# Performance work log

Measured on AMD Instinct MI355X. Metric: run time of the kernel, lower is better.

The kernel has to match this reference:

```python
import jax, jax.numpy as jnp
import numpy as np

B, T, DIM = 8, 2048, 512
DM, EXPAND, NSTATE, HDIM, L = 128, 2, 16, 64, 2
DINNER = DM * EXPAND            # 256
NH = DINNER // HDIM             # 4 heads
CONVDIM = DINNER + 2 * NSTATE   # 288 (n_groups=1)
PROJ = DINNER + CONVDIM + NH    # 548
K = 4                           # conv kernel (HF default)
EPS = 1e-5


def setup_inputs() -> dict:
    key = jax.random.key(0)
    ks = jax.random.split(key, 8)
    s = 0.02
    return {
        "x": jax.random.normal(ks[0], (B, T, DIM), jnp.float32),
        "in_w": jax.random.normal(ks[1], (DIM, DM), jnp.float32) * s,
        "in_b": jnp.zeros((DM,), jnp.float32),
        "norm_w": jnp.ones((L, DM), jnp.float32),
        "inproj_w": jax.random.normal(ks[2], (L, DM, PROJ), jnp.float32) * s,
        "conv_w": jax.random.normal(ks[3], (L, CONVDIM, 1, K), jnp.float32) * 0.2,
        "conv_b": jnp.zeros((L, CONVDIM), jnp.float32),
        "A_log": jnp.log(jax.random.uniform(ks[4], (L, NH), jnp.float32, 1.0, 8.0)),
        "D": jnp.ones((L, NH), jnp.float32),
        "dt_bias": jnp.log(jnp.expm1(jax.random.uniform(ks[5], (L, NH), jnp.float32, 1e-3, 0.1))),
        "gnorm_w": jnp.ones((L, DINNER), jnp.float32),
        "outproj_w": jax.random.normal(ks[6], (L, DINNER, DM), jnp.float32) * s,
        "normf_w": jnp.ones((DM,), jnp.float32),
        "out_w": jax.random.normal(ks[7], (DM, DIM), jnp.float32) * s,
        "out_b": jnp.zeros((DIM,), jnp.float32),
    }


def _rmsnorm(x, w):
    var = jnp.mean(x * x, axis=-1, keepdims=True)
    return x * jax.lax.rsqrt(var + EPS) * w


def _gated_rmsnorm(y, gate, w):
    y = y * jax.nn.silu(gate)
    var = jnp.mean(y * y, axis=-1, keepdims=True)
    return y * jax.lax.rsqrt(var + EPS) * w


def _causal_conv(h, w, b):
    # h: [B,T,C] depthwise causal conv, kernel K, left pad K-1
    out = jax.lax.conv_general_dilated(
        h.swapaxes(1, 2), w, (1,), [(K - 1, 0)],
        feature_group_count=CONVDIM,
        dimension_numbers=("NCH", "OIH", "NCH"))
    return out.swapaxes(1, 2) + b


def _ssd(xs, dt, A, Bm, Cm, Dh):
    # selective state-space scan (math-equivalent to HF Mamba2 chunked SSD)
    # xs [B,T,H,P], dt [B,T,H], A [H], Bm/Cm [B,T,N], Dh [H]
    dA = jnp.exp(dt * A)  # [B,T,H]

    def step(state, inp):
        dA_t, dt_t, x_t, B_t, C_t = inp
        dBx = dt_t[:, :, None, None] * x_t[..., None] * B_t[:, None, None, :]
        state = state * dA_t[:, :, None, None] + dBx  # [B,H,P,N]
        y = jnp.einsum("bhpn,bn->bhp", state, C_t)
        return state, y

    init = jnp.zeros((xs.shape[0], NH, HDIM, NSTATE), xs.dtype)
    _, ys = jax.lax.scan(step, init, (dA.swapaxes(0, 1), dt.swapaxes(0, 1),
                                      xs.swapaxes(0, 1), Bm.swapaxes(0, 1), Cm.swapaxes(0, 1)))
    return ys.swapaxes(0, 1) + xs * Dh[None, None, :, None]


def reference(x, in_w, in_b, norm_w, inproj_w, conv_w, conv_b, A_log, D,
              dt_bias, gnorm_w, outproj_w, normf_w, out_w, out_b):
    h = x @ in_w + in_b  # [B,T,DM]
    for l in range(L):
        res = h
        hn = _rmsnorm(h, norm_w[l])
        proj = hn @ inproj_w[l]  # [B,T,PROJ]
        gate = proj[..., :DINNER]
        hBC = proj[..., DINNER:DINNER + CONVDIM]
        dt = proj[..., DINNER + CONVDIM:]
        hBC = jax.nn.silu(_causal_conv(hBC, conv_w[l], conv_b[l]))
        xs = hBC[..., :DINNER].reshape(B, T, NH, HDIM)
        Bm = hBC[..., DINNER:DINNER + NSTATE]
        Cm = hBC[..., DINNER + NSTATE:]
        A = -jnp.exp(A_log[l])
        dt = jax.nn.softplus(dt + dt_bias[l])  # time_step_limit=(0,inf): no clamp
        y = _ssd(xs, dt, A, Bm, Cm, D[l]).reshape(B, T, DINNER)
        y = _gated_rmsnorm(y, gate, gnorm_w[l])
        h = res + y @ outproj_w[l]
    h = _rmsnorm(h, normf_w)
    pooled = h.mean(axis=1)  # mean pool over T
    return pooled @ out_w + out_b
```

## Files before the change

### kernel.cpp

```cpp
#include <hip/hip_runtime.h>
#include <math.h>

typedef unsigned short ushort_t;
typedef unsigned int uint_t;

#define B_      8
#define T_      2048
#define DIMX    512
#define DM      128
#define DINNER  256
#define NSTATE  16
#define HDIM    64
#define NH      4
#define CONVDIM 288
#define PROJ    548
#define KCONV   4
#define LLAYERS 2
#define QCH     128
#define NC      (T_/QCH)
#define EPSF    1e-5f
#define MTOK    (B_*T_)

#define OFF_H      0u
#define OFF_PROJ   2097152u
#define OFF_HBC    11075584u
#define OFF_Y      15794176u
#define OFF_DTP    19988480u
#define OFF_CUM    20054016u
#define OFF_Z      20119552u
#define OFF_SPREV  20643840u
#define OFF_DEC    21168128u
#define OFF_PART   21168640u
#define OFF_BF     21299712u
#define OFF_WTIN   23396864u
#define OFF_WTINP  23429632u
#define OFF_WTOUT  23503360u

__device__ __forceinline__ ushort_t f2b(float f) {
    uint_t u = __builtin_bit_cast(uint_t, f);
    return (ushort_t)((u + 0x7FFFu + ((u >> 16) & 1u)) >> 16);
}
__device__ __forceinline__ float b2f(ushort_t b) {
    uint_t u = ((uint_t)b) << 16;
    return __builtin_bit_cast(float, u);
}

typedef short bf8 __attribute__((ext_vector_type(8)));
typedef float f4v __attribute__((ext_vector_type(4)));

__global__ __launch_bounds__(256) void k_wt_all(
    const float* __restrict__ in_w, const float* __restrict__ inproj_w,
    const float* __restrict__ outproj_w,
    ushort_t* __restrict__ wt_in, ushort_t* __restrict__ wt_inp,
    ushort_t* __restrict__ wt_out)
{
    __shared__ float tile[64][65];
    int idx = blockIdx.x;
    const float* W; ushort_t* Wt; int K, N, k0, n0;
    if (idx < 16) {
        W = in_w; Wt = wt_in; K = 512; N = 128;
        k0 = (idx & 7) * 64; n0 = (idx >> 3) * 64;
    } else if (idx < 52) {
        int r = idx - 16; int l = r / 18; r -= l * 18;
        W = inproj_w + l * 128 * PROJ; Wt = wt_inp + l * 576 * 128; K = 128; N = PROJ;
        k0 = (r & 1) * 64; n0 = (r >> 1) * 64;
    } else {
        int r = idx - 52; int l = r / 8; r -= l * 8;
        W = outproj_w + l * 256 * 128; Wt = wt_out + l * 128 * 256; K = 256; N = 128;
        k0 = (r & 3) * 64; n0 = (r >> 2) * 64;
    }
    const int tid = threadIdx.x;
#pragma unroll
    for (int it = 0; it < 16; ++it) {
        const int e = it * 256 + tid;
        const int kk = e >> 6, nn = e & 63;
        tile[kk][nn] = (n0 + nn < N) ? W[(k0 + kk) * N + (n0 + nn)] : 0.f;
    }
    __syncthreads();
#pragma unroll
    for (int it = 0; it < 16; ++it) {
        const int e = it * 256 + tid;
        const int nn = e >> 6, kk = e & 63;
        Wt[(n0 + nn) * K + k0 + kk] = f2b(tile[kk][nn]);
    }
}

template<int KTOT, int LDC, int NGUARD, int EPI, bool ABF16>
__global__ __launch_bounds__(256) void k_gemm(
    const void* __restrict__ Ap, const ushort_t* __restrict__ Bt,
    const float* __restrict__ aux, float* __restrict__ C)
{
    __shared__ ushort_t Als[64 * 136];
    __shared__ ushort_t Bls[64 * 136];
    const int m0 = blockIdx.x * 64, n0 = blockIdx.y * 64;
    const int tid = threadIdx.x;
    const int lane = tid & 63, w = tid >> 6;
    const int wm = (w >> 1) * 32, wn = (w & 1) * 32;
    const int r16 = lane & 15, q8 = (lane >> 4) * 8;

    f4v acc[2][2];
#pragma unroll
    for (int i = 0; i < 2; ++i)
#pragma unroll
        for (int j = 0; j < 2; ++j) acc[i][j] = (f4v)0.f;

    for (int kc = 0; kc < KTOT; kc += 128) {
        if constexpr (ABF16) {
            const ushort_t* A = (const ushort_t*)Ap;
#pragma unroll
            for (int i = 0; i < 4; ++i) {
                const int e = i * 2048 + tid * 8;
                const int r = e >> 7, c = e & 127;
                *(uint4*)&Als[r * 136 + c] = *(const uint4*)&A[(m0 + r) * KTOT + kc + c];
            }
        } else {
            const float* A = (const float*)Ap;
#pragma unroll
            for (int i = 0; i < 4; ++i) {
                const int e = i * 2048 + tid * 8;
                const int r = e >> 7, c = e & 127;
                const float4 f0 = *(const float4*)&A[(m0 + r) * KTOT + kc + c];
                const float4 f1 = *(const float4*)&A[(m0 + r) * KTOT + kc + c + 4];
                uint4 pk;
                pk.x = (uint_t)f2b(f0.x) | ((uint_t)f2b(f0.y) << 16);
                pk.y = (uint_t)f2b(f0.z) | ((uint_t)f2b(f0.w) << 16);
                pk.z = (uint_t)f2b(f1.x) | ((uint_t)f2b(f1.y) << 16);
                pk.w = (uint_t)f2b(f1.z) | ((uint_t)f2b(f1.w) << 16);
                *(uint4*)&Als[r * 136 + c] = pk;
            }
        }
#pragma unroll
        for (int i = 0; i < 4; ++i) {
            const int e = i * 2048 + tid * 8;
            const int r = e >> 7, c = e & 127;
            *(uint4*)&Bls[r * 136 + c] = *(const uint4*)&Bt[(n0 + r) * KTOT + kc + c];
        }
        __syncthreads();
#pragma unroll
        for (int kk = 0; kk < 128; kk += 32) {
            const bf8 a0 = *(const bf8*)&Als[(wm + r16) * 136 + kk + q8];
            const bf8 a1 = *(const bf8*)&Als[(wm + 16 + r16) * 136 + kk + q8];
            const bf8 b0 = *(const bf8*)&Bls[(wn + r16) * 136 + kk + q8];
            const bf8 b1 = *(const bf8*)&Bls[(wn + 16 + r16) * 136 + kk + q8];
            acc[0][0] = __builtin_amdgcn_mfma_f32_16x16x32_bf16(a0, b0, acc[0][0], 0, 0, 0);
            acc[0][1] = __builtin_amdgcn_mfma_f32_16x16x32_bf16(a0, b1, acc[0][1], 0, 0, 0);
            acc[1][0] = __builtin_amdgcn_mfma_f32_16x16x32_bf16(a1, b0, acc[1][0], 0, 0, 0);
            acc[1][1] = __builtin_amdgcn_mfma_f32_16x16x32_bf16(a1, b1, acc[1][1], 0, 0, 0);
        }
        __syncthreads();
    }
    const int q4 = (lane >> 4) * 4;
#pragma unroll
    for (int i = 0; i < 2; ++i)
#pragma unroll
        for (int j = 0; j < 2; ++j)
#pragma unroll
            for (int r = 0; r < 4; ++r) {
                const int grow = m0 + wm + i * 16 + q4 + r;
                const int gcol = n0 + wn + j * 16 + r16;
                if (NGUARD == 0 || gcol < NGUARD) {
                    float v = acc[i][j][r];
                    if (EPI == 1) v += aux[gcol];
                    if (EPI == 2) v += C[grow * LDC + gcol];
                    C[grow * LDC + gcol] = v;
                }
            }
}

__global__ __launch_bounds__(256) void k_gemm_rms(
    const float* __restrict__ h, const float* __restrict__ nw,
    const ushort_t* __restrict__ Bt, float* __restrict__ C)
{
    __shared__ ushort_t Als[64 * 136];
    __shared__ ushort_t Bls[64 * 136];
    const int m0 = blockIdx.x * 64, n0 = blockIdx.y * 64;
    const int tid = threadIdx.x;
    const int lane = tid & 63, w = tid >> 6;
    const int wm = (w >> 1) * 32, wn = (w & 1) * 32;
    const int r16 = lane & 15, q8 = (lane >> 4) * 8;

#pragma unroll
    for (int i = 0; i < 4; ++i) {
        const int e = i * 2048 + tid * 8;
        const int r = e >> 7, c = e & 127;
        const float4 f0 = *(const float4*)&h[(m0 + r) * 128 + c];
        const float4 f1 = *(const float4*)&h[(m0 + r) * 128 + c + 4];
        float ss = f0.x * f0.x + f0.y * f0.y + f0.z * f0.z + f0.w * f0.w
                 + f1.x * f1.x + f1.y * f1.y + f1.z * f1.z + f1.w * f1.w;
#pragma unroll
        for (int off = 1; off < 16; off <<= 1) ss += __shfl_xor(ss, off);
        const float rs = rsqrtf(ss * (1.f / 128.f) + EPSF);
        const float4 w0 = *(const float4*)&nw[c];
        const float4 w1 = *(const float4*)&nw[c + 4];
        uint4 pk;
        pk.x = (uint_t)f2b(f0.x * rs * w0.x) | ((uint_t)f2b(f0.y * rs * w0.y) << 16);
        pk.y = (uint_t)f2b(f0.z * rs * w0.z) | ((uint_t)f2b(f0.w * rs * w0.w) << 16);
        pk.z = (uint_t)f2b(f1.x * rs * w1.x) | ((uint_t)f2b(f1.y * rs * w1.y) << 16);
        pk.w = (uint_t)f2b(f1.z * rs * w1.z) | ((uint_t)f2b(f1.w * rs * w1.w) << 16);
        *(uint4*)&Als[r * 136 + c] = pk;
    }
#pragma unroll
    for (int i = 0; i < 4; ++i) {
        const int e = i * 2048 + tid * 8;
        const int r = e >> 7, c = e & 127;
        *(uint4*)&Bls[r * 136 + c] = *(const uint4*)&Bt[(n0 + r) * 128 + c];
    }
    __syncthreads();

    f4v acc[2][2];
#pragma unroll
    for (int i = 0; i < 2; ++i)
#pragma unroll
        for (int j = 0; j < 2; ++j) acc[i][j] = (f4v)0.f;
#pragma unroll
    for (int kk = 0; kk < 128; kk += 32) {
        const bf8 a0 = *(const bf8*)&Als[(wm + r16) * 136 + kk + q8];
        const bf8 a1 = *(const bf8*)&Als[(wm + 16 + r16) * 136 + kk + q8];
        const bf8 b0 = *(const bf8*)&Bls[(wn + r16) * 136 + kk + q8];
        const bf8 b1 = *(const bf8*)&Bls[(wn + 16 + r16) * 136 + kk + q8];
        acc[0][0] = __builtin_amdgcn_mfma_f32_16x16x32_bf16(a0, b0, acc[0][0], 0, 0, 0);
        acc[0][1] = __builtin_amdgcn_mfma_f32_16x16x32_bf16(a0, b1, acc[0][1], 0, 0, 0);
        acc[1][0] = __builtin_amdgcn_mfma_f32_16x16x32_bf16(a1, b0, acc[1][0], 0, 0, 0);
        acc[1][1] = __builtin_amdgcn_mfma_f32_16x16x32_bf16(a1, b1, acc[1][1], 0, 0, 0);
    }

    const int q4 = (lane >> 4) * 4;
#pragma unroll
    for (int i = 0; i < 2; ++i)
#pragma unroll
        for (int j = 0; j < 2; ++j)
#pragma unroll
            for (int r = 0; r < 4; ++r) {
                const int grow = m0 + wm + i * 16 + q4 + r;
                const int gcol = n0 + wn + j * 16 + r16;
                if (gcol < PROJ) C[grow * PROJ + gcol] = acc[i][j][r];
            }
}

__global__ __launch_bounds__(256) void k_gemm_gn(
    const float* __restrict__ y, const float* __restrict__ proj,
    const float* __restrict__ gw, const ushort_t* __restrict__ Bt,
    float* __restrict__ C)
{
    __shared__ ushort_t Als[64 * 264];
    __shared__ ushort_t Bls[64 * 136];
    const int m0 = blockIdx.x * 64, n0 = blockIdx.y * 64;
    const int tid = threadIdx.x;
    const int lane = tid & 63, w = tid >> 6;
    const int wm = (w >> 1) * 32, wn = (w & 1) * 32;
    const int r16 = lane & 15, q8 = (lane >> 4) * 8;

#pragma unroll
    for (int i = 0; i < 8; ++i) {
        const int e = i * 2048 + tid * 8;
        const int r = e >> 8, c = e & 255;
        const float4 y0 = *(const float4*)&y[(m0 + r) * 256 + c];
        const float4 y1 = *(const float4*)&y[(m0 + r) * 256 + c + 4];
        const float4 g0 = *(const float4*)&proj[(m0 + r) * PROJ + c];
        const float4 g1 = *(const float4*)&proj[(m0 + r) * PROJ + c + 4];
        float v0 = y0.x * (g0.x / (1.f + __expf(-g0.x)));
        float v1 = y0.y * (g0.y / (1.f + __expf(-g0.y)));
        float v2 = y0.z * (g0.z / (1.f + __expf(-g0.z)));
        float v3 = y0.w * (g0.w / (1.f + __expf(-g0.w)));
        float v4 = y1.x * (g1.x / (1.f + __expf(-g1.x)));
        float v5 = y1.y * (g1.y / (1.f + __expf(-g1.y)));
        float v6 = y1.z * (g1.z / (1.f + __expf(-g1.z)));
        float v7 = y1.w * (g1.w / (1.f + __expf(-g1.w)));
        float ss = v0 * v0 + v1 * v1 + v2 * v2 + v3 * v3
                 + v4 * v4 + v5 * v5 + v6 * v6 + v7 * v7;
#pragma unroll
        for (int off = 1; off < 32; off <<= 1) ss += __shfl_xor(ss, off);
        const float rs = rsqrtf(ss * (1.f / 256.f) + EPSF);
        const float4 w0 = *(const float4*)&gw[c];
        const float4 w1 = *(const float4*)&gw[c + 4];
        uint4 pk;
        pk.x = (uint_t)f2b(v0 * rs * w0.x) | ((uint_t)f2b(v1 * rs * w0.y) << 16);
        pk.y = (uint_t)f2b(v2 * rs * w0.z) | ((uint_t)f2b(v3 * rs * w0.w) << 16);
        pk.z = (uint_t)f2b(v4 * rs * w1.x) | ((uint_t)f2b(v5 * rs * w1.y) << 16);
        pk.w = (uint_t)f2b(v6 * rs * w1.z) | ((uint_t)f2b(v7 * rs * w1.w) << 16);
        *(uint4*)&Als[r * 264 + c] = pk;
    }

    f4v acc[2][2];
#pragma unroll
    for (int i = 0; i < 2; ++i)
#pragma unroll
        for (int j = 0; j < 2; ++j) acc[i][j] = (f4v)0.f;

    for (int kc = 0; kc < 256; kc += 128) {
#pragma unroll
        for (int i = 0; i < 4; ++i) {
            const int e = i * 2048 + tid * 8;
            const int r = e >> 7, c = e & 127;
            *(uint4*)&Bls[r * 136 + c] = *(const uint4*)&Bt[(n0 + r) * 256 + kc + c];
        }
        __syncthreads();
#pragma unroll
        for (int kk = 0; kk < 128; kk += 32) {
            const bf8 a0 = *(const bf8*)&Als[(wm + r16) * 264 + kc + kk + q8];
            const bf8 a1 = *(const bf8*)&Als[(wm + 16 + r16) * 264 + kc + kk + q8];
            const bf8 b0 = *(const bf8*)&Bls[(wn + r16) * 136 + kk + q8];
            const bf8 b1 = *(const bf8*)&Bls[(wn + 16 + r16) * 136 + kk + q8];
            acc[0][0] = __builtin_amdgcn_mfma_f32_16x16x32_bf16(a0, b0, acc[0][0], 0, 0, 0);
            acc[0][1] = __builtin_amdgcn_mfma_f32_16x16x32_bf16(a0, b1, acc[0][1], 0, 0, 0);
            acc[1][0] = __builtin_amdgcn_mfma_f32_16x16x32_bf16(a1, b0, acc[1][0], 0, 0, 0);
            acc[1][1] = __builtin_amdgcn_mfma_f32_16x16x32_bf16(a1, b1, acc[1][1], 0, 0, 0);
        }
        __syncthreads();
    }

    const int q4 = (lane >> 4) * 4;
#pragma unroll
    for (int i = 0; i < 2; ++i)
#pragma unroll
        for (int j = 0; j < 2; ++j)
#pragma unroll
            for (int r = 0; r < 4; ++r) {
                const int grow = m0 + wm + i * 16 + q4 + r;
                const int gcol = n0 + wn + j * 16 + r16;
                C[grow * 128 + gcol] += acc[i][j][r];
            }
}

__global__ __launch_bounds__(256) void k_convdt(
    const float* __restrict__ proj, const float* __restrict__ cw,
    const float* __restrict__ cb, const float* __restrict__ A_log,
    const float* __restrict__ dt_bias, float* __restrict__ hbc,
    float* __restrict__ dtp, float* __restrict__ cum, int l)
{
    __shared__ float sc[128];
    const int bid = blockIdx.x;
    const int tid = threadIdx.x;
    if (bid < (MTOK * CONVDIM) / 256) {
        const int e = bid * 256 + tid;
        const int m = e / CONVDIM;
        const int cch = e - m * CONVDIM;
        const int b = m >> 11;
        const int t = m & (T_ - 1);
        const float* wp = cw + (l * CONVDIM + cch) * KCONV;
        float acc = cb[l * CONVDIM + cch];
#pragma unroll
        for (int k = 0; k < KCONV; ++k) {
            const int tt = t - (KCONV - 1) + k;
            if (tt >= 0) acc += proj[(b * T_ + tt) * PROJ + DINNER + cch] * wp[k];
        }
        hbc[m * CONVDIM + cch] = acc / (1.f + __expf(-acc));
    } else {
        const int bid2 = bid - (MTOK * CONVDIM) / 256;
        const int c = bid2 & (NC - 1);
        const int hh = (bid2 / NC) & (NH - 1);
        const int b = bid2 / (NC * NH);
        const int t = tid;
        float dtv = 0.f;
        if (t < 128) {
            const int m = b * T_ + c * QCH + t;
            const float Ah = -expf(A_log[l * NH + hh]);
            const float raw = proj[m * PROJ + DINNER + CONVDIM + hh] + dt_bias[l * NH + hh];
            dtv = (raw > 20.f) ? raw : log1pf(expf(raw));
            sc[t] = dtv * Ah;
        }
        __syncthreads();
        for (int off = 1; off < 128; off <<= 1) {
            const float v = (t >= off && t < 128) ? sc[t - off] : 0.f;
            __syncthreads();
            if (t < 128) sc[t] += v;
            __syncthreads();
        }
        if (t < 128) {
            const int m = b * T_ + c * QCH + t;
            dtp[m * NH + hh] = dtv;
            cum[m * NH + hh] = sc[t];
        }
    }
}

__global__ __launch_bounds__(256) void k_ssd_state(
    const float* __restrict__ hbc, const float* __restrict__ dtp,
    const float* __restrict__ cum, float* __restrict__ zbuf,
    float* __restrict__ dec)
{
    __shared__ ushort_t Xt[64 * 136];
    __shared__ ushort_t wB[16 * 136];
    __shared__ float cumls[QCH];
    __shared__ float dtls[QCH];
    const int bid = blockIdx.x;
    const int c = bid & (NC - 1);
    const int hh = (bid / NC) & (NH - 1);
    const int b = bid / (NC * NH);
    const int m0 = b * T_ + c * QCH;
    const int tid = threadIdx.x;

    if (tid < QCH) {
        cumls[tid] = cum[(m0 + tid) * NH + hh];
        dtls[tid] = dtp[(m0 + tid) * NH + hh];
    }
    __syncthreads();
    const float clast = cumls[QCH - 1];
    {
        const int p = tid & 63;
        const int s0 = tid >> 6;
#pragma unroll
        for (int pass = 0; pass < 32; ++pass) {
            const int s = s0 + pass * 4;
            Xt[p * 136 + s] = f2b(hbc[(m0 + s) * CONVDIM + hh * 64 + p]);
        }
    }
    for (int e = tid; e < QCH * 16; e += 256) {
        const int n = e & 15, s = e >> 4;
        const float w = __expf(clast - cumls[s]) * dtls[s];
        wB[n * 136 + s] = f2b(w * hbc[(m0 + s) * CONVDIM + DINNER + n]);
    }
    __syncthreads();

    const int lane = tid & 63, w = tid >> 6;
    const int r16 = lane & 15, q8 = (lane >> 4) * 8, q4 = (lane >> 4) * 4;
    f4v acc = (f4v)0.f;
#pragma unroll
    for (int kc = 0; kc < 128; kc += 32) {
        const bf8 a = *(const bf8*)&Xt[(w * 16 + r16) * 136 + kc + q8];
        const bf8 bb = *(const bf8*)&wB[r16 * 136 + kc + q8];
        acc = __builtin_amdgcn_mfma_f32_16x16x32_bf16(a, bb, acc, 0, 0, 0);
    }
#pragma unroll
    for (int r = 0; r < 4; ++r) {
        const int p = w * 16 + q4 + r;
        zbuf[bid * 1024 + p * 16 + r16] = acc[r];
    }
    if (tid == 0) dec[bid] = __expf(clast);
}

__global__ __launch_bounds__(256) void k_ssd_y(
    const float* __restrict__ hbc, const float* __restrict__ dtp,
    const float* __restrict__ cum, const float* __restrict__ zbuf,
    const float* __restrict__ dec, const float* __restrict__ Dvec,
    float* __restrict__ ybuf, int l)
{
    __shared__ ushort_t Xt[64 * 136];
    __shared__ ushort_t BlsT[128 * 40];
    __shared__ ushort_t ClsT[128 * 40];
    __shared__ ushort_t Gls[128 * 136];
    __shared__ ushort_t Spt[64 * 40];
    __shared__ float cumls[QCH];
    __shared__ float dtls[QCH];
    const int bid = blockIdx.x;
    const int c = bid & (NC - 1);
    const int hh = (bid / NC) & (NH - 1);
    const int b = bid / (NC * NH);
    const int bh = bid >> 4;
    const int m0 = b * T_ + c * QCH;
    const int tid = threadIdx.x;

    if (tid < QCH) {
        cumls[tid] = cum[(m0 + tid) * NH + hh];
        dtls[tid] = dtp[(m0 + tid) * NH + hh];
    }
    {
        const int p = tid & 63;
        const int s0 = tid >> 6;
#pragma unroll
        for (int pass = 0; pass < 32; ++pass) {
            const int s = s0 + pass * 4;
            Xt[p * 136 + s] = f2b(hbc[(m0 + s) * CONVDIM + hh * 64 + p]);
        }
    }
    for (int e = tid; e < QCH * 16; e += 256) {
        const int n = e & 15, s = e >> 4;
        BlsT[s * 40 + n] = f2b(hbc[(m0 + s) * CONVDIM + DINNER + n]);
        BlsT[s * 40 + 16 + n] = 0;
        ClsT[s * 40 + n] = f2b(hbc[(m0 + s) * CONVDIM + DINNER + NSTATE + n]);
        ClsT[s * 40 + 16 + n] = 0;
    }
    {
        float4 S; S.x = 0.f; S.y = 0.f; S.z = 0.f; S.w = 0.f;
        for (int cc = 0; cc < c; ++cc) {
            const float d = dec[bh * NC + cc];
            const float4 z = *(const float4*)(zbuf + (bh * NC + cc) * 1024 + tid * 4);
            S.x = S.x * d + z.x; S.y = S.y * d + z.y;
            S.z = S.z * d + z.z; S.w = S.w * d + z.w;
        }
        const int p = tid >> 2, n = (tid & 3) * 4;
        Spt[p * 40 + n]     = f2b(S.x);
        Spt[p * 40 + n + 1] = f2b(S.y);
        Spt[p * 40 + n + 2] = f2b(S.z);
        Spt[p * 40 + n + 3] = f2b(S.w);
        Spt[p * 40 + 16 + n]     = 0;
        Spt[p * 40 + 16 + n + 1] = 0;
        Spt[p * 40 + 16 + n + 2] = 0;
        Spt[p * 40 + 16 + n + 3] = 0;
    }
    __syncthreads();

    const int lane = tid & 63, w = tid >> 6;
    const int wrow = w * 32;
    const int r16 = lane & 15, q8 = (lane >> 4) * 8, q4 = (lane >> 4) * 4;
    const float Dh = Dvec[l * NH + hh];

    bf8 cfr[2];
#pragma unroll
    for (int i = 0; i < 2; ++i)
        cfr[i] = *(const bf8*)&ClsT[(wrow + i * 16 + r16) * 40 + q8];

    float cumt[8], et[8];
#pragma unroll
    for (int i = 0; i < 2; ++i)
#pragma unroll
        for (int r = 0; r < 4; ++r) {
            const int t = wrow + i * 16 + q4 + r;
            cumt[i * 4 + r] = cumls[t];
            et[i * 4 + r] = __expf(cumls[t]);
        }

    f4v acc[2][4];
#pragma unroll
    for (int j = 0; j < 4; ++j) {
        const bf8 sf = *(const bf8*)&Spt[(j * 16 + r16) * 40 + q8];
#pragma unroll
        for (int i = 0; i < 2; ++i) {
            f4v z = (f4v)0.f;
            z = __builtin_amdgcn_mfma_f32_16x16x32_bf16(cfr[i], sf, z, 0, 0, 0);
#pragma unroll
            for (int r = 0; r < 4; ++r) {
                const int t = wrow + i * 16 + q4 + r;
                const int p = j * 16 + r16;
                acc[i][j][r] = z[r] * et[i * 4 + r] + Dh * b2f(Xt[p * 136 + t]);
            }
        }
    }

#pragma unroll
    for (int ts = 0; ts < 8; ++ts) {
        const bf8 bf = *(const bf8*)&BlsT[(ts * 16 + r16) * 40 + q8];
        const int s = ts * 16 + r16;
        const float cs = cumls[s];
        const float ds = dtls[s];
#pragma unroll
        for (int i = 0; i < 2; ++i) {
            f4v g = (f4v)0.f;
            g = __builtin_amdgcn_mfma_f32_16x16x32_bf16(cfr[i], bf, g, 0, 0, 0);
#pragma unroll
            for (int r = 0; r < 4; ++r) {
                const int t = wrow + i * 16 + q4 + r;
                const float val = (s <= t) ? __expf(cumt[i * 4 + r] - cs) * ds * g[r] : 0.f;
                Gls[t * 136 + s] = f2b(val);
            }
        }
    }
    __syncthreads();

#pragma unroll
    for (int kc = 0; kc < 128; kc += 32) {
        bf8 af[2];
#pragma unroll
        for (int i = 0; i < 2; ++i)
            af[i] = *(const bf8*)&Gls[(wrow + i * 16 + r16) * 136 + kc + q8];
#pragma unroll
        for (int j = 0; j < 4; ++j) {
            const bf8 xf = *(const bf8*)&Xt[(j * 16 + r16) * 136 + kc + q8];
#pragma unroll
            for (int i = 0; i < 2; ++i)
                acc[i][j] = __builtin_amdgcn_mfma_f32_16x16x32_bf16(af[i], xf, acc[i][j], 0, 0, 0);
        }
    }

#pragma unroll
    for (int i = 0; i < 2; ++i)
#pragma unroll
        for (int r = 0; r < 4; ++r) {
            const int t = wrow + i * 16 + q4 + r;
#pragma unroll
            for (int j = 0; j < 4; ++j) {
                const int p = j * 16 + r16;
                ybuf[(m0 + t) * DINNER + hh * 64 + p] = acc[i][j][r];
            }
        }
}

__global__ __launch_bounds__(256) void k_finalnorm_pool(
    const float* __restrict__ h, const float* __restrict__ nfw,
    float* __restrict__ part)
{
    __shared__ float ht[2048];
    __shared__ float red[256];
    __shared__ float rstd[16];
    __shared__ float padd[256];
    const int tile = blockIdx.x & 127;
    const int b = blockIdx.x >> 7;
    const int m0 = b * T_ + tile * 16;
    const int tid = threadIdx.x;
    for (int e = tid; e < 2048; e += 256) ht[e] = h[m0 * DM + e];
    __syncthreads();
    {
        const int tg = tid >> 4, j0 = tid & 15;
        float p = 0.f;
#pragma unroll
        for (int k = 0; k < 8; ++k) { const float v = ht[tg * 128 + j0 + 16 * k]; p += v * v; }
        red[tid] = p;
    }
    __syncthreads();
    if (tid < 16) {
        float s = 0.f;
#pragma unroll
        for (int q = 0; q < 16; ++q) s += red[tid * 16 + q];
        rstd[tid] = rsqrtf(s * (1.f / 128.f) + EPSF);
    }
    __syncthreads();
    const int d = tid & 127, half = tid >> 7;
    float ps = 0.f;
#pragma unroll
    for (int i0 = 0; i0 < 8; ++i0) { const int i = half + 2 * i0; ps += ht[i * 128 + d] * rstd[i]; }
    padd[tid] = ps;
    __syncthreads();
    if (tid < 128) part[(b * 128 + tile) * 128 + tid] = (padd[tid] + padd[128 + tid]) * nfw[tid];
}

__global__ __launch_bounds__(256) void k_head(
    const float* __restrict__ part, const float* __restrict__ ow,
    const float* __restrict__ ob, float* __restrict__ out)
{
    __shared__ float pooled[128];
    const int b = blockIdx.x;
    const int tid = threadIdx.x;
    if (tid < 128) {
        float s = 0.f;
        for (int tile = 0; tile < 128; ++tile) s += part[(b * 128 + tile) * 128 + tid];
        pooled[tid] = s * (1.f / (float)T_);
    }
    __syncthreads();
    for (int o = tid; o < DIMX; o += 256) {
        float acc = ob[o];
#pragma unroll 4
        for (int d = 0; d < 128; ++d) acc += pooled[d] * ow[d * DIMX + o];
        out[b * DIMX + o] = acc;
    }
}

extern "C" void kernel_launch(void* const* d_in, const int* in_sizes, int n_in,
                              void* d_out, int out_size, void* d_ws, size_t ws_size,
                              hipStream_t stream)
{
    const float* x         = (const float*)d_in[0];
    const float* in_w      = (const float*)d_in[1];
    const float* in_b      = (const float*)d_in[2];
    const float* norm_w    = (const float*)d_in[3];
    const float* inproj_w  = (const float*)d_in[4];
    const float* conv_w    = (const float*)d_in[5];
    const float* conv_b    = (const float*)d_in[6];
    const float* A_log     = (const float*)d_in[7];
    const float* Dvec      = (const float*)d_in[8];
    const float* dt_bias   = (const float*)d_in[9];
    const float* gnorm_w   = (const float*)d_in[10];
    const float* outproj_w = (const float*)d_in[11];
    const float* normf_w   = (const float*)d_in[12];
    const float* out_w     = (const float*)d_in[13];
    const float* out_b     = (const float*)d_in[14];

    float* ws    = (float*)d_ws;
    float* h     = ws + OFF_H;
    float* proj  = ws + OFF_PROJ;
    float* hbc   = ws + OFF_HBC;
    float* ybuf  = ws + OFF_Y;
    float* dtp   = ws + OFF_DTP;
    float* cumb  = ws + OFF_CUM;
    float* zbuf  = ws + OFF_Z;
    float* dec   = ws + OFF_DEC;
    float* part  = ws + OFF_PART;
    ushort_t* wt_in  = (ushort_t*)(ws + OFF_WTIN);
    ushort_t* wt_inp = (ushort_t*)(ws + OFF_WTINP);
    ushort_t* wt_out = (ushort_t*)(ws + OFF_WTOUT);

    k_wt_all<<<68, 256, 0, stream>>>(in_w, inproj_w, outproj_w, wt_in, wt_inp, wt_out);

    k_gemm<512, 128, 0, 1, false><<<dim3(MTOK / 64, 2), 256, 0, stream>>>(x, wt_in, in_b, h);

    for (int l = 0; l < LLAYERS; ++l) {
        k_gemm_rms<<<dim3(MTOK / 64, 9), 256, 0, stream>>>(
            h, norm_w + l * DM, wt_inp + l * 576 * 128, proj);
        k_convdt<<<(MTOK * CONVDIM) / 256 + B_ * NH * NC, 256, 0, stream>>>(
            proj, conv_w, conv_b, A_log, dt_bias, hbc, dtp, cumb, l);
        k_ssd_state<<<B_ * NH * NC, 256, 0, stream>>>(hbc, dtp, cumb, zbuf, dec);
        k_ssd_y<<<B_ * NH * NC, 256, 0, stream>>>(hbc, dtp, cumb, zbuf, dec, Dvec, ybuf, l);
        k_gemm_gn<<<dim3(MTOK / 64, 2), 256, 0, stream>>>(
            ybuf, proj, gnorm_w + l * DINNER, wt_out + l * 128 * 256, h);
    }

    k_finalnorm_pool<<<B_ * (T_ / 16), 256, 0, stream>>>(h, normf_w, part);
    k_head<<<B_, 256, 0, stream>>>(part, out_w, out_b, (float*)d_out);
}
```

Baseline: 299.3 us.

## Store proj, hbc and y intermediates in bf16 to cut memory traffic

Converts the main inter-kernel activations (projection output, conv/SiLU output, SSD output) from fp32 to bf16 storage, keeping dt in a separate small fp32 buffer. The projection row stride drops from 548 to 544 so gate and hBC columns stay aligned for vector loads. This roughly halves global memory traffic between the GEMM, conv, SSD and gated-norm kernels, and it removes bf16 conversions that the SSD kernels did on load. In exchange the gate and y values lose precision before the SiLU and gated norm.

```diff
diff --git a/kernel.cpp b/kernel.cpp
--- a/kernel.cpp
+++ b/kernel.cpp
@@ -22,19 +22,18 @@
 #define MTOK    (B_*T_)
 
 #define OFF_H      0u
-#define OFF_PROJ   2097152u
-#define OFF_HBC    11075584u
-#define OFF_Y      15794176u
 #define OFF_DTP    19988480u
 #define OFF_CUM    20054016u
 #define OFF_Z      20119552u
-#define OFF_SPREV  20643840u
 #define OFF_DEC    21168128u
 #define OFF_PART   21168640u
-#define OFF_BF     21299712u
 #define OFF_WTIN   23396864u
 #define OFF_WTINP  23429632u
 #define OFF_WTOUT  23503360u
+#define OFF_PROJB  23600000u
+#define OFF_DTRAW  28100000u
+#define OFF_HBCB   28200000u
+#define OFF_YB     30600000u
 
 __device__ __forceinline__ ushort_t f2b(float f) {
     uint_t u = __builtin_bit_cast(uint_t, f);
@@ -44,6 +43,8 @@
     uint_t u = ((uint_t)b) << 16;
     return __builtin_bit_cast(float, u);
 }
+__device__ __forceinline__ float blo(uint_t u) { return b2f((ushort_t)(u & 0xffffu)); }
+__device__ __forceinline__ float bhi(uint_t u) { return b2f((ushort_t)(u >> 16)); }
 
 typedef short bf8 __attribute__((ext_vector_type(8)));
 typedef float f4v __attribute__((ext_vector_type(4)));
@@ -169,7 +170,8 @@
 
 __global__ __launch_bounds__(256) void k_gemm_rms(
     const float* __restrict__ h, const float* __restrict__ nw,
-    const ushort_t* __restrict__ Bt, float* __restrict__ C)
+    const ushort_t* __restrict__ Bt, ushort_t* __restrict__ projb,
+    float* __restrict__ dtraw)
 {
     __shared__ ushort_t Als[64 * 136];
     __shared__ ushort_t Bls[64 * 136];
@@ -233,12 +235,13 @@
             for (int r = 0; r < 4; ++r) {
                 const int grow = m0 + wm + i * 16 + q4 + r;
                 const int gcol = n0 + wn + j * 16 + r16;
-                if (gcol < PROJ) C[grow * PROJ + gcol] = acc[i][j][r];
+                if (gcol < 544) projb[grow * 544 + gcol] = f2b(acc[i][j][r]);
+                else if (gcol < PROJ) dtraw[grow * 4 + (gcol - 544)] = acc[i][j][r];
             }
 }
 
 __global__ __launch_bounds__(256) void k_gemm_gn(
-    const float* __restrict__ y, const float* __restrict__ proj,
+    const ushort_t* __restrict__ yb, const ushort_t* __restrict__ projb,
     const float* __restrict__ gw, const ushort_t* __restrict__ Bt,
     float* __restrict__ C)
 {
@@ -254,18 +257,18 @@
     for (int i = 0; i < 8; ++i) {
         const int e = i * 2048 + tid * 8;
         const int r = e >> 8, c = e & 255;
-        const float4 y0 = *(const float4*)&y[(m0 + r) * 256 + c];
-        const float4 y1 = *(const float4*)&y[(m0 + r) * 256 + c + 4];
-        const float4 g0 = *(const float4*)&proj[(m0 + r) * PROJ + c];
-        const float4 g1 = *(const float4*)&proj[(m0 + r) * PROJ + c + 4];
-        float v0 = y0.x * (g0.x / (1.f + __expf(-g0.x)));
-        float v1 = y0.y * (g0.y / (1.f + __expf(-g0.y)));
-        float v2 = y0.z * (g0.z / (1.f + __expf(-g0.z)));
-        float v3 = y0.w * (g0.w / (1.f + __expf(-g0.w)));
-        float v4 = y1.x * (g1.x / (1.f + __expf(-g1.x)));
-        float v5 = y1.y * (g1.y / (1.f + __expf(-g1.y)));
-        float v6 = y1.z * (g1.z / (1.f + __expf(-g1.z)));
-        float v7 = y1.w * (g1.w / (1.f + __expf(-g1.w)));
+        const uint4 yv = *(const uint4*)&yb[(m0 + r) * 256 + c];
+        const uint4 gv = *(const uint4*)&projb[(m0 + r) * 544 + c];
+        const float g0 = blo(gv.x), g1 = bhi(gv.x), g2 = blo(gv.y), g3 = bhi(gv.y);
+        const float g4 = blo(gv.z), g5 = bhi(gv.z), g6 = blo(gv.w), g7 = bhi(gv.w);
+        float v0 = blo(yv.x) * (g0 / (1.f + __expf(-g0)));
+        float v1 = bhi(yv.x) * (g1 / (1.f + __expf(-g1)));
+        float v2 = blo(yv.y) * (g2 / (1.f + __expf(-g2)));
+        float v3 = bhi(yv.y) * (g3 / (1.f + __expf(-g3)));
+        float v4 = blo(yv.z) * (g4 / (1.f + __expf(-g4)));
+        float v5 = bhi(yv.z) * (g5 / (1.f + __expf(-g5)));
+        float v6 = blo(yv.w) * (g6 / (1.f + __expf(-g6)));
+        float v7 = bhi(yv.w) * (g7 / (1.f + __expf(-g7)));
         float ss = v0 * v0 + v1 * v1 + v2 * v2 + v3 * v3
                  + v4 * v4 + v5 * v5 + v6 * v6 + v7 * v7;
 #pragma unroll
@@ -323,10 +326,11 @@
 }
 
 __global__ __launch_bounds__(256) void k_convdt(
-    const float* __restrict__ proj, const float* __restrict__ cw,
-    const float* __restrict__ cb, const float* __restrict__ A_log,
-    const float* __restrict__ dt_bias, float* __restrict__ hbc,
-    float* __restrict__ dtp, float* __restrict__ cum, int l)
+    const ushort_t* __restrict__ projb, const float* __restrict__ dtraw,
+    const float* __restrict__ cw, const float* __restrict__ cb,
+    const float* __restrict__ A_log, const float* __restrict__ dt_bias,
+    ushort_t* __restrict__ hbcb, float* __restrict__ dtp,
+    float* __restrict__ cum, int l)
 {
     __shared__ float sc[128];
     const int bid = blockIdx.x;
@@ -342,9 +346,9 @@
 #pragma unroll
         for (int k = 0; k < KCONV; ++k) {
             const int tt = t - (KCONV - 1) + k;
-            if (tt >= 0) acc += proj[(b * T_ + tt) * PROJ + DINNER + cch] * wp[k];
-        }
-        hbc[m * CONVDIM + cch] = acc / (1.f + __expf(-acc));
+            if (tt >= 0) acc += b2f(projb[(b * T_ + tt) * 544 + 256 + cch]) * wp[k];
+        }
+        hbcb[m * CONVDIM + cch] = f2b(acc / (1.f + __expf(-acc)));
     } else {
         const int bid2 = bid - (MTOK * CONVDIM) / 256;
         const int c = bid2 & (NC - 1);
@@ -355,7 +359,7 @@
         if (t < 128) {
             const int m = b * T_ + c * QCH + t;
             const float Ah = -expf(A_log[l * NH + hh]);
-            const float raw = proj[m * PROJ + DINNER + CONVDIM + hh] + dt_bias[l * NH + hh];
+            const float raw = dtraw[m * 4 + hh] + dt_bias[l * NH + hh];
             dtv = (raw > 20.f) ? raw : log1pf(expf(raw));
             sc[t] = dtv * Ah;
         }
@@ -375,7 +379,7 @@
 }
 
 __global__ __launch_bounds__(256) void k_ssd_state(
-    const float* __restrict__ hbc, const float* __restrict__ dtp,
+    const ushort_t* __restrict__ hbcb, const float* __restrict__ dtp,
     const float* __restrict__ cum, float* __restrict__ zbuf,
     float* __restrict__ dec)
 {
@@ -402,13 +406,13 @@
 #pragma unroll
         for (int pass = 0; pass < 32; ++pass) {
             const int s = s0 + pass * 4;
-            Xt[p * 136 + s] = f2b(hbc[(m0 + s) * CONVDIM + hh * 64 + p]);
+            Xt[p * 136 + s] = hbcb[(m0 + s) * CONVDIM + hh * 64 + p];
         }
     }
     for (int e = tid; e < QCH * 16; e += 256) {
         const int n = e & 15, s = e >> 4;
         const float w = __expf(clast - cumls[s]) * dtls[s];
-        wB[n * 136 + s] = f2b(w * hbc[(m0 + s) * CONVDIM + DINNER + n]);
+        wB[n * 136 + s] = f2b(w * b2f(hbcb[(m0 + s) * CONVDIM + DINNER + n]));
     }
     __syncthreads();
 
@@ -430,10 +434,10 @@
 }
 
 __global__ __launch_bounds__(256) void k_ssd_y(
-    const float* __restrict__ hbc, const float* __restrict__ dtp,
+    const ushort_t* __restrict__ hbcb, const float* __restrict__ dtp,
     const float* __restrict__ cum, const float* __restrict__ zbuf,
     const float* __restrict__ dec, const float* __restrict__ Dvec,
-    float* __restrict__ ybuf, int l)
+    ushort_t* __restrict__ yb, int l)
 {
     __shared__ ushort_t Xt[64 * 136];
     __shared__ ushort_t BlsT[128 * 40];
@@ -460,14 +464,14 @@
 #pragma unroll
         for (int pass = 0; pass < 32; ++pass) {
             const int s = s0 + pass * 4;
-            Xt[p * 136 + s] = f2b(hbc[(m0 + s) * CONVDIM + hh * 64 + p]);
+            Xt[p * 136 + s] = hbcb[(m0 + s) * CONVDIM + hh * 64 + p];
         }
     }
     for (int e = tid; e < QCH * 16; e += 256) {
         const int n = e & 15, s = e >> 4;
-        BlsT[s * 40 + n] = f2b(hbc[(m0 + s) * CONVDIM + DINNER + n]);
+        BlsT[s * 40 + n] = hbcb[(m0 + s) * CONVDIM + DINNER + n];
         BlsT[s * 40 + 16 + n] = 0;
-        ClsT[s * 40 + n] = f2b(hbc[(m0 + s) * CONVDIM + DINNER + NSTATE + n]);
+        ClsT[s * 40 + n] = hbcb[(m0 + s) * CONVDIM + DINNER + NSTATE + n];
         ClsT[s * 40 + 16 + n] = 0;
     }
     {
@@ -570,7 +574,7 @@
 #pragma unroll
             for (int j = 0; j < 4; ++j) {
                 const int p = j * 16 + r16;
-                ybuf[(m0 + t) * DINNER + hh * 64 + p] = acc[i][j][r];
+                yb[(m0 + t) * DINNER + hh * 64 + p] = f2b(acc[i][j][r]);
             }
         }
 }
@@ -656,14 +660,15 @@
 
     float* ws    = (float*)d_ws;
     float* h     = ws + OFF_H;
-    float* proj  = ws + OFF_PROJ;
-    float* hbc   = ws + OFF_HBC;
-    float* ybuf  = ws + OFF_Y;
     float* dtp   = ws + OFF_DTP;
     float* cumb  = ws + OFF_CUM;
     float* zbuf  = ws + OFF_Z;
     float* dec   = ws + OFF_DEC;
     float* part  = ws + OFF_PART;
+    float* dtraw = ws + OFF_DTRAW;
+    ushort_t* projb = (ushort_t*)(ws + OFF_PROJB);
+    ushort_t* hbcb  = (ushort_t*)(ws + OFF_HBCB);
+    ushort_t* yb    = (ushort_t*)(ws + OFF_YB);
     ushort_t* wt_in  = (ushort_t*)(ws + OFF_WTIN);
     ushort_t* wt_inp = (ushort_t*)(ws + OFF_WTINP);
     ushort_t* wt_out = (ushort_t*)(ws + OFF_WTOUT);
@@ -674,13 +679,13 @@
 
     for (int l = 0; l < LLAYERS; ++l) {
         k_gemm_rms<<<dim3(MTOK / 64, 9), 256, 0, stream>>>(
-            h, norm_w + l * DM, wt_inp + l * 576 * 128, proj);
+            h, norm_w + l * DM, wt_inp + l * 576 * 128, projb, dtraw);
         k_convdt<<<(MTOK * CONVDIM) / 256 + B_ * NH * NC, 256, 0, stream>>>(
-            proj, conv_w, conv_b, A_log, dt_bias, hbc, dtp, cumb, l);
-        k_ssd_state<<<B_ * NH * NC, 256, 0, stream>>>(hbc, dtp, cumb, zbuf, dec);
-        k_ssd_y<<<B_ * NH * NC, 256, 0, stream>>>(hbc, dtp, cumb, zbuf, dec, Dvec, ybuf, l);
+            projb, dtraw, conv_w, conv_b, A_log, dt_bias, hbcb, dtp, cumb, l);
+        k_ssd_state<<<B_ * NH * NC, 256, 0, stream>>>(hbcb, dtp, cumb, zbuf, dec);
+        k_ssd_y<<<B_ * NH * NC, 256, 0, stream>>>(hbcb, dtp, cumb, zbuf, dec, Dvec, yb, l);
         k_gemm_gn<<<dim3(MTOK / 64, 2), 256, 0, stream>>>(
-            ybuf, proj, gnorm_w + l * DINNER, wt_out + l * 128 * 256, h);
+            yb, projb, gnorm_w + l * DINNER, wt_out + l * 128 * 256, h);
     }
 
     k_finalnorm_pool<<<B_ * (T_ / 16), 256, 0, stream>>>(h, normf_w, part);
```

After: 277.4 us. 7.3% less time.
